# Kernel tuning notes

Measured on AMD Instinct MI355X. Metric: run time of the kernel, lower is better.

## Reference

```python
import jax, jax.numpy as jnp
import numpy as np

MARGIN = 0.5          # TripletLoss(margin=0.5)
N_FEAT = 100000       # gallery size N (rows of `features`)
D = 128               # embedding dim
N_BATCH = 256         # batch size n
N_CLASSES = 1000      # number of identities -> ~100 positives per class


def setup_inputs() -> dict:
    key = jax.random.key(0)
    k1, k2 = jax.random.split(key)
    inputs = jax.random.normal(k1, (N_BATCH, D), dtype=jnp.float32)
    features = jax.random.normal(k2, (N_FEAT, D), dtype=jnp.float32)
    # feature_labels encodes the t2i dict: label of every gallery row.
    feature_labels = (jnp.arange(N_FEAT, dtype=jnp.int32) % N_CLASSES).astype(jnp.int32)
    # idx[i] is the gallery row corresponding to batch sample i (distinct rows).
    idx = jnp.arange(N_BATCH, dtype=jnp.int32)
    # consistency: targets[i] must equal feature_labels[idx[i]]
    targets = feature_labels[idx]
    return {"inputs": inputs, "features": features, "targets": targets,
            "feature_labels": feature_labels, "idx": idx}


def reference(inputs, features, targets, feature_labels, idx):
    # sim_mat = inputs @ features.T  -> [n, N]
    sim = jnp.matmul(inputs, features.T)
    n_feat = features.shape[0]
    # pos: same identity, excluding the sample's own gallery row idx[i]
    same = feature_labels[None, :] == targets[:, None]          # [n, N]
    is_self = jnp.arange(n_feat, dtype=idx.dtype)[None, :] == idx[:, None]
    pos_mask = same & ~is_self
    neg_mask = ~same
    big = jnp.asarray(jnp.finfo(sim.dtype).max, sim.dtype)
    pos = jnp.min(jnp.where(pos_mask, sim, big), axis=1)        # hardest positive (min sim)
    neg = jnp.max(jnp.where(neg_mask, sim, -big), axis=1)       # hardest negative (max sim)
    loss = jax.nn.relu(neg - pos + MARGIN)                      # [n]
    return jnp.sum(loss) / targets.shape[0]
```

## Files before the change

### kernel.cpp

```cpp
#include <hip/hip_runtime.h>

#define NFEAT   100000
#define NBATCH  256
#define DIM     128
#define MARGIN_F 0.5f
#define GRID    625
#define IPB     10
#define CROWS   16
#define ROWS_PB (IPB * CROWS)
#define NBUF    4
#define CBYTES  (CROWS * DIM * 4)
#define FLT_BIG 3.402823466e+38f

typedef __bf16 bf8_t  __attribute__((ext_vector_type(8)));
typedef short  sh8_t  __attribute__((ext_vector_type(8)));
typedef float  f32x4  __attribute__((ext_vector_type(4)));

__device__ __forceinline__ bf8_t pack8(float4 v0, float4 v1) {
  bf8_t r;
  r[0] = (__bf16)v0.x; r[1] = (__bf16)v0.y; r[2] = (__bf16)v0.z; r[3] = (__bf16)v0.w;
  r[4] = (__bf16)v1.x; r[5] = (__bf16)v1.y; r[6] = (__bf16)v1.z; r[7] = (__bf16)v1.w;
  return r;
}

template <typename VA, typename VC>
__device__ __forceinline__ auto mfma_sel(VA a, VA b, VC c, int)
    -> decltype(__builtin_amdgcn_mfma_f32_16x16x32_bf16(a, b, c, 0, 0, 0)) {
  return __builtin_amdgcn_mfma_f32_16x16x32_bf16(a, b, c, 0, 0, 0);
}
template <typename VA, typename VC>
__device__ __forceinline__ VC mfma_sel(VA a, VA b, VC c, long) {
  return __builtin_amdgcn_mfma_f32_16x16x32_bf16(
      __builtin_bit_cast(sh8_t, a), __builtin_bit_cast(sh8_t, b), c, 0, 0, 0);
}
__device__ __forceinline__ f32x4 mfma_bf16(bf8_t a, bf8_t b, f32x4 c) {
  return mfma_sel(a, b, c, 0);
}

#if defined(__has_builtin)
#if __has_builtin(__builtin_amdgcn_global_load_lds)
#define HAVE_GLLDS 1
#endif
#endif

__device__ __forceinline__ void stage16(const char* g, char* l) {
#ifdef HAVE_GLLDS
  __builtin_amdgcn_global_load_lds(
      (const __attribute__((address_space(1))) unsigned int*)g,
      (__attribute__((address_space(3))) unsigned int*)l, 16, 0, 0);
#else
  *reinterpret_cast<float4*>(l) = *reinterpret_cast<const float4*>(g);
#endif
}

#define WAITVM(N) asm volatile("s_waitcnt vmcnt(" #N ")" ::: "memory")
#define CFENCE()  asm volatile("" ::: "memory")

__global__ __launch_bounds__(512, 2) void triplet_partial(
    const float* __restrict__ inputs, const float* __restrict__ features,
    const int* __restrict__ targets, const int* __restrict__ flabels,
    const int* __restrict__ idx,
    float* __restrict__ ppos, float* __restrict__ pneg,
    float* __restrict__ out)
{
  __shared__ char sbuf[NBUF][CBYTES];
  __shared__ int  slab[ROWS_PB];

  const int tid  = threadIdx.x;
  const int lane = tid & 63;
  const int wv   = tid >> 6;
  const int l15  = lane & 15;
  const int lg   = lane >> 4;
  const int m0   = wv * 32;
  const int blk  = blockIdx.x;
  const int rowbase = blk * ROWS_PB;

  if (blk == 0 && tid == 0) out[0] = 0.0f;

  auto stage_chunk = [&](int buf, int c) {
    const int p    = tid * 16;
    const int prow = p >> 9;
    const int srow = rowbase + c * CROWS + prow;
    const int scol = (p & 511) ^ ((prow & 7) << 4);
    stage16((const char*)features + (size_t)srow * 512 + scol, &sbuf[buf][p]);
  };

  bf8_t afrag[2][4];
#pragma unroll
  for (int mt = 0; mt < 2; ++mt) {
    const float* ap = inputs + (m0 + mt * 16 + l15) * DIM;
    float4 v0[4], v1[4];
#pragma unroll
    for (int ks = 0; ks < 4; ++ks) {
      const int k = ks * 32 + lg * 8;
      v0[ks] = *reinterpret_cast<const float4*>(ap + k);
      v1[ks] = *reinterpret_cast<const float4*>(ap + k + 4);
    }
#pragma unroll
    for (int ks = 0; ks < 4; ++ks)
      afrag[mt][ks] = pack8(v0[ks], v1[ks]);
  }

  int meta[2][4];
#pragma unroll
  for (int mt = 0; mt < 2; ++mt)
#pragma unroll
    for (int rr = 0; rr < 4; ++rr) {
      const int row = m0 + mt * 16 + lg * 4 + rr;
      meta[mt][rr] = (idx[row] << 10) | targets[row];
    }

  int labv = 0;
  if (tid < ROWS_PB) labv = flabels[rowbase + tid];

  stage_chunk(0, 0); stage_chunk(1, 1); stage_chunk(2, 2);

  if (tid < ROWS_PB) slab[tid] = labv;

  float minpos[2][4], maxneg[2][4];
#pragma unroll
  for (int mt = 0; mt < 2; ++mt)
#pragma unroll
    for (int rr = 0; rr < 4; ++rr) { minpos[mt][rr] = FLT_BIG; maxneg[mt][rr] = -FLT_BIG; }

  asm volatile("s_waitcnt lgkmcnt(0)" ::: "memory");
  __builtin_amdgcn_s_barrier();
  CFENCE();

#pragma unroll
  for (int c = 0; c < IPB; ++c) {
    if (c < IPB - 2)      { WAITVM(2); }
    else if (c == IPB - 2){ WAITVM(1); }
    else                  { WAITVM(0); }
    __builtin_amdgcn_s_barrier();
    CFENCE();

    if (c + 3 < IPB) stage_chunk((c + 3) & 3, c + 3);

    const int jcol = c * CROWS + l15;
    const int j    = rowbase + jcol;
    const int labj = slab[jcol];

    bf8_t bfrag[4];
    const char* rbase = &sbuf[c & 3][l15 * 512];
    const int   swz   = (l15 & 7) << 4;
#pragma unroll
    for (int ks = 0; ks < 4; ++ks) {
      const int b0 = ks * 128 + lg * 32;
      float4 v0 = *reinterpret_cast<const float4*>(rbase + ((b0)      ^ swz));
      float4 v1 = *reinterpret_cast<const float4*>(rbase + ((b0 + 16) ^ swz));
      bfrag[ks] = pack8(v0, v1);
    }

#pragma unroll
    for (int mt = 0; mt < 2; ++mt) {
      f32x4 acc = {0.f, 0.f, 0.f, 0.f};
#pragma unroll
      for (int ks = 0; ks < 4; ++ks)
        acc = mfma_bf16(afrag[mt][ks], bfrag[ks], acc);
#pragma unroll
      for (int rr = 0; rr < 4; ++rr) {
        const float s    = acc[rr];
        const int   m    = meta[mt][rr];
        const bool same  = (labj == (m & 1023));
        const bool self  = (j == (m >> 10));
        minpos[mt][rr] = fminf(minpos[mt][rr], (same && !self) ? s : FLT_BIG);
        maxneg[mt][rr] = fmaxf(maxneg[mt][rr], same ? -FLT_BIG : s);
      }
    }
  }

#pragma unroll
  for (int mt = 0; mt < 2; ++mt)
#pragma unroll
    for (int rr = 0; rr < 4; ++rr) {
      float mp = minpos[mt][rr], mn = maxneg[mt][rr];
#pragma unroll
      for (int m = 1; m < 16; m <<= 1) {
        mp = fminf(mp, __shfl_xor(mp, m, 64));
        mn = fmaxf(mn, __shfl_xor(mn, m, 64));
      }
      if (l15 == 0) {
        const int row = m0 + mt * 16 + lg * 4 + rr;
        ppos[blk * NBATCH + row] = mp;
        pneg[blk * NBATCH + row] = mn;
      }
    }
}

__global__ __launch_bounds__(256) void triplet_reduce(
    const float* __restrict__ ppos, const float* __restrict__ pneg,
    float* __restrict__ out)
{
  const int r = blockIdx.x;
  const int t = threadIdx.x;
  float mp = FLT_BIG, mn = -FLT_BIG;
  for (int b = t; b < GRID; b += 256) {
    mp = fminf(mp, ppos[b * NBATCH + r]);
    mn = fmaxf(mn, pneg[b * NBATCH + r]);
  }
#pragma unroll
  for (int m = 1; m < 64; m <<= 1) {
    mp = fminf(mp, __shfl_xor(mp, m, 64));
    mn = fmaxf(mn, __shfl_xor(mn, m, 64));
  }
  __shared__ float smp[4], smn[4];
  if ((t & 63) == 0) { smp[t >> 6] = mp; smn[t >> 6] = mn; }
  __syncthreads();
  if (t == 0) {
    mp = fminf(fminf(smp[0], smp[1]), fminf(smp[2], smp[3]));
    mn = fmaxf(fmaxf(smn[0], smn[1]), fmaxf(smn[2], smn[3]));
    float loss = mn - mp + MARGIN_F;
    loss = loss > 0.f ? loss : 0.f;
    atomicAdd(out, loss * (1.0f / NBATCH));
  }
}

extern "C" void kernel_launch(void* const* d_in, const int* in_sizes, int n_in,
                              void* d_out, int out_size, void* d_ws, size_t ws_size,
                              hipStream_t stream) {
  const float* inputs   = (const float*)d_in[0];
  const float* features = (const float*)d_in[1];
  const int*   targets  = (const int*)d_in[2];
  const int*   flabels  = (const int*)d_in[3];
  const int*   idx      = (const int*)d_in[4];
  float* out  = (float*)d_out;
  float* ppos = (float*)d_ws;
  float* pneg = ppos + (size_t)GRID * NBATCH;

  triplet_partial<<<GRID, 512, 0, stream>>>(inputs, features, targets, flabels, idx, ppos, pneg, out);
  triplet_reduce<<<NBATCH, 256, 0, stream>>>(ppos, pneg, out);
}
```

Baseline: 47.16 us.

## Replace in-block pipelining with one-shot staging and more, smaller blocks

Each block now covers 80 gallery rows and loads them all into LDS in a single burst with one barrier, instead of streaming 16-row chunks through a 4-deep ring buffer with waitcnt and barriers per chunk. The grid doubles to 1250 blocks, and launch bounds ask for 4 blocks per CU, so latency is hidden by occupancy rather than by software pipelining. Labels now come from registers, and the partial-result layout is transposed so the reduce kernel reads contiguous memory. The cost is twice as many partial results to reduce, plus the per-block setup (loading the A fragments and meta values) repeated across more blocks.

```diff
diff --git a/kernel.cpp b/kernel.cpp
--- a/kernel.cpp
+++ b/kernel.cpp
@@ -4,12 +4,10 @@
 #define NBATCH  256
 #define DIM     128
 #define MARGIN_F 0.5f
-#define GRID    625
-#define IPB     10
-#define CROWS   16
-#define ROWS_PB (IPB * CROWS)
-#define NBUF    4
-#define CBYTES  (CROWS * DIM * 4)
+#define GRID    1250
+#define RPB     80
+#define NTILE   5
+#define BBYTES  (RPB * DIM * 4)
 #define FLT_BIG 3.402823466e+38f
 
 typedef __bf16 bf8_t  __attribute__((ext_vector_type(8)));
@@ -53,18 +51,14 @@
 #endif
 }
 
-#define WAITVM(N) asm volatile("s_waitcnt vmcnt(" #N ")" ::: "memory")
-#define CFENCE()  asm volatile("" ::: "memory")
-
-__global__ __launch_bounds__(512, 2) void triplet_partial(
+__global__ __launch_bounds__(512, 4) void triplet_partial(
     const float* __restrict__ inputs, const float* __restrict__ features,
     const int* __restrict__ targets, const int* __restrict__ flabels,
     const int* __restrict__ idx,
     float* __restrict__ ppos, float* __restrict__ pneg,
     float* __restrict__ out)
 {
-  __shared__ char sbuf[NBUF][CBYTES];
-  __shared__ int  slab[ROWS_PB];
+  __shared__ char sB[BBYTES];
 
   const int tid  = threadIdx.x;
   const int lane = tid & 63;
@@ -73,17 +67,18 @@
   const int lg   = lane >> 4;
   const int m0   = wv * 32;
   const int blk  = blockIdx.x;
-  const int rowbase = blk * ROWS_PB;
+  const int rowbase = blk * RPB;
 
   if (blk == 0 && tid == 0) out[0] = 0.0f;
 
-  auto stage_chunk = [&](int buf, int c) {
-    const int p    = tid * 16;
+#pragma unroll
+  for (int i = 0; i < NTILE; ++i) {
+    const int p    = i * 8192 + tid * 16;
     const int prow = p >> 9;
-    const int srow = rowbase + c * CROWS + prow;
     const int scol = (p & 511) ^ ((prow & 7) << 4);
-    stage16((const char*)features + (size_t)srow * 512 + scol, &sbuf[buf][p]);
-  };
+    stage16((const char*)features + (size_t)(rowbase + prow) * 512 + scol,
+            &sB[p]);
+  }
 
   bf8_t afrag[2][4];
 #pragma unroll
@@ -101,6 +96,11 @@
       afrag[mt][ks] = pack8(v0[ks], v1[ks]);
   }
 
+  int lab[NTILE];
+#pragma unroll
+  for (int t = 0; t < NTILE; ++t)
+    lab[t] = flabels[rowbase + t * 16 + l15];
+
   int meta[2][4];
 #pragma unroll
   for (int mt = 0; mt < 2; ++mt)
@@ -110,62 +110,48 @@
       meta[mt][rr] = (idx[row] << 10) | targets[row];
     }
 
-  int labv = 0;
-  if (tid < ROWS_PB) labv = flabels[rowbase + tid];
-
-  stage_chunk(0, 0); stage_chunk(1, 1); stage_chunk(2, 2);
-
-  if (tid < ROWS_PB) slab[tid] = labv;
-
   float minpos[2][4], maxneg[2][4];
 #pragma unroll
   for (int mt = 0; mt < 2; ++mt)
 #pragma unroll
     for (int rr = 0; rr < 4; ++rr) { minpos[mt][rr] = FLT_BIG; maxneg[mt][rr] = -FLT_BIG; }
 
-  asm volatile("s_waitcnt lgkmcnt(0)" ::: "memory");
-  __builtin_amdgcn_s_barrier();
-  CFENCE();
-
-#pragma unroll
-  for (int c = 0; c < IPB; ++c) {
-    if (c < IPB - 2)      { WAITVM(2); }
-    else if (c == IPB - 2){ WAITVM(1); }
-    else                  { WAITVM(0); }
-    __builtin_amdgcn_s_barrier();
-    CFENCE();
-
-    if (c + 3 < IPB) stage_chunk((c + 3) & 3, c + 3);
-
-    const int jcol = c * CROWS + l15;
-    const int j    = rowbase + jcol;
-    const int labj = slab[jcol];
-
-    bf8_t bfrag[4];
-    const char* rbase = &sbuf[c & 3][l15 * 512];
-    const int   swz   = (l15 & 7) << 4;
+  __syncthreads();
+
+  const int swz = (l15 & 7) << 4;
+#pragma unroll
+  for (int t = 0; t < NTILE; ++t) {
+    const char* rbase = &sB[(t * 16 + l15) * 512];
+    const int   j     = rowbase + t * 16 + l15;
+    const int   labj  = lab[t];
+
+    f32x4 acc0 = {0.f, 0.f, 0.f, 0.f};
+    f32x4 acc1 = {0.f, 0.f, 0.f, 0.f};
 #pragma unroll
     for (int ks = 0; ks < 4; ++ks) {
-      const int b0 = ks * 128 + lg * 32;
-      float4 v0 = *reinterpret_cast<const float4*>(rbase + ((b0)      ^ swz));
-      float4 v1 = *reinterpret_cast<const float4*>(rbase + ((b0 + 16) ^ swz));
-      bfrag[ks] = pack8(v0, v1);
-    }
-
-#pragma unroll
-    for (int mt = 0; mt < 2; ++mt) {
-      f32x4 acc = {0.f, 0.f, 0.f, 0.f};
-#pragma unroll
-      for (int ks = 0; ks < 4; ++ks)
-        acc = mfma_bf16(afrag[mt][ks], bfrag[ks], acc);
-#pragma unroll
-      for (int rr = 0; rr < 4; ++rr) {
-        const float s    = acc[rr];
-        const int   m    = meta[mt][rr];
+      const int o = ks * 128 + lg * 32;
+      float4 v0 = *reinterpret_cast<const float4*>(rbase + ((o)      ^ swz));
+      float4 v1 = *reinterpret_cast<const float4*>(rbase + ((o + 16) ^ swz));
+      bf8_t bf = pack8(v0, v1);
+      acc0 = mfma_bf16(afrag[0][ks], bf, acc0);
+      acc1 = mfma_bf16(afrag[1][ks], bf, acc1);
+    }
+
+#pragma unroll
+    for (int rr = 0; rr < 4; ++rr) {
+      {
+        const int   m    = meta[0][rr];
         const bool same  = (labj == (m & 1023));
         const bool self  = (j == (m >> 10));
-        minpos[mt][rr] = fminf(minpos[mt][rr], (same && !self) ? s : FLT_BIG);
-        maxneg[mt][rr] = fmaxf(maxneg[mt][rr], same ? -FLT_BIG : s);
+        minpos[0][rr] = fminf(minpos[0][rr], (same && !self) ? acc0[rr] : FLT_BIG);
+        maxneg[0][rr] = fmaxf(maxneg[0][rr], same ? -FLT_BIG : acc0[rr]);
+      }
+      {
+        const int   m    = meta[1][rr];
+        const bool same  = (labj == (m & 1023));
+        const bool self  = (j == (m >> 10));
+        minpos[1][rr] = fminf(minpos[1][rr], (same && !self) ? acc1[rr] : FLT_BIG);
+        maxneg[1][rr] = fmaxf(maxneg[1][rr], same ? -FLT_BIG : acc1[rr]);
       }
     }
   }
@@ -182,8 +168,8 @@
       }
       if (l15 == 0) {
         const int row = m0 + mt * 16 + lg * 4 + rr;
-        ppos[blk * NBATCH + row] = mp;
-        pneg[blk * NBATCH + row] = mn;
+        ppos[row * GRID + blk] = mp;
+        pneg[row * GRID + blk] = mn;
       }
     }
 }
@@ -196,8 +182,8 @@
   const int t = threadIdx.x;
   float mp = FLT_BIG, mn = -FLT_BIG;
   for (int b = t; b < GRID; b += 256) {
-    mp = fminf(mp, ppos[b * NBATCH + r]);
-    mn = fmaxf(mn, pneg[b * NBATCH + r]);
+    mp = fminf(mp, ppos[r * GRID + b]);
+    mn = fmaxf(mn, pneg[r * GRID + b]);
   }
 #pragma unroll
   for (int m = 1; m < 64; m <<= 1) {
@@ -226,7 +212,7 @@
   const int*   idx      = (const int*)d_in[4];
   float* out  = (float*)d_out;
   float* ppos = (float*)d_ws;
-  float* pneg = ppos + (size_t)GRID * NBATCH;
+  float* pneg = ppos + (size_t)NBATCH * GRID;
 
   triplet_partial<<<GRID, 512, 0, stream>>>(inputs, features, targets, flabels, idx, ppos, pneg, out);
   triplet_reduce<<<NBATCH, 256, 0, stream>>>(ppos, pneg, out);
```

New measurement: 44.74 us. -5.1%, faster.
